# Kernel optimization log

Measured on AMD Instinct MI355X. Metric: run time of the kernel, lower is better.

Reference implementation:

```python
import jax, jax.numpy as jnp
import numpy as np

MEM_DIM = 4000
FEATURES = 2048
THRESHOLD = 1.0 / MEM_DIM
EPS = 1e-12
COS_EPS = 1e-8  # torch CosineSimilarity default eps


def setup_inputs() -> dict:
    key = jax.random.key(0)
    k1, k2 = jax.random.split(key)
    x = jax.random.normal(k1, (8192, FEATURES), dtype=jnp.float32)
    # kaiming_uniform_ with a=0: bound = sqrt(6 / fan_in), fan_in = FEATURES
    bound = float(np.sqrt(6.0 / FEATURES))
    memory = jax.random.uniform(k2, (MEM_DIM, FEATURES), dtype=jnp.float32,
                                minval=-bound, maxval=bound)
    return {"x": x, "memory": memory}


def reference(x, memory):
    # Cosine similarity via normalized matmul: [b, MEM_DIM]
    z_norm = jnp.linalg.norm(x, axis=1)              # [b]
    m_norm = jnp.linalg.norm(memory, axis=1)         # [M]
    logits = (x @ memory.T) / jnp.maximum(z_norm[:, None] * m_norm[None, :], COS_EPS)
    w = jax.nn.softmax(logits, axis=1)               # [b, M]
    # sparse shrinkage: relu(w - t) * w / (|w - t| + eps)
    d = w - THRESHOLD
    w = jnp.maximum(d, 0.0) * w / (jnp.abs(d) + EPS)
    # L1 normalize over memory dim (F.normalize p=1, eps=1e-12)
    w = w / jnp.maximum(jnp.sum(jnp.abs(w), axis=1, keepdims=True), EPS)
    return w @ memory                                # [b, features]
```

## Files before the change

### kernel.cpp

```cpp
#include <hip/hip_runtime.h>
#include <hip/hip_fp16.h>
#include <math.h>

#define FEATURES 2048
#define MROWS 4000
#define NPAD 4096
#define BROWS 8192

typedef unsigned short u16;
typedef unsigned int u32;

typedef __attribute__((ext_vector_type(8))) _Float16 f16x8;
typedef __attribute__((ext_vector_type(8))) short s16x8;
typedef __attribute__((ext_vector_type(4))) float f32x4;

__device__ __forceinline__ u16 f2h(float f) {
  union { _Float16 h; u16 u; } cv;
  cv.h = (_Float16)f;
  return cv.u;
}
__device__ __forceinline__ u16 f2bf(float f) {
  u32 u = __float_as_uint(f);
  u32 r = (u + 0x7FFFu + ((u >> 16) & 1u)) >> 16;
  return (u16)r;
}
__device__ __forceinline__ float bf2f(u16 h) {
  return __uint_as_float(((u32)h) << 16);
}

#define GLD16(g, l)                                                            \
  __builtin_amdgcn_global_load_lds(                                            \
      (const __attribute__((address_space(1))) u32*)(g),                       \
      (__attribute__((address_space(3))) u32*)(l), 16, 0, 0)


__global__ __launch_bounds__(256) void conv_split_bf16_kernel(
    const float* __restrict__ src, u16* __restrict__ hi, u16* __restrict__ lo,
    float* __restrict__ norms, int nrows) {
  __shared__ float red[4];
  const int row = blockIdx.x;
  const int tid = threadIdx.x;
  ushort4* hp = (ushort4*)(hi + (size_t)row * FEATURES);
  ushort4* lp = (ushort4*)(lo + (size_t)row * FEATURES);
  float ss = 0.f;
  if (row < nrows) {
    const float4* sp = (const float4*)(src + (size_t)row * FEATURES);
#pragma unroll
    for (int p = 0; p < 2; ++p) {
      const int idx = tid + p * 256;
      float4 f = sp[idx];
      ushort4 h, l;
      h.x = f2bf(f.x); l.x = f2bf(f.x - bf2f(h.x)); ss += f.x * f.x;
      h.y = f2bf(f.y); l.y = f2bf(f.y - bf2f(h.y)); ss += f.y * f.y;
      h.z = f2bf(f.z); l.z = f2bf(f.z - bf2f(h.z)); ss += f.z * f.z;
      h.w = f2bf(f.w); l.w = f2bf(f.w - bf2f(h.w)); ss += f.w * f.w;
      hp[idx] = h;
      lp[idx] = l;
    }
  } else {
    const ushort4 zz = {0, 0, 0, 0};
#pragma unroll
    for (int p = 0; p < 2; ++p) {
      hp[tid + p * 256] = zz;
      lp[tid + p * 256] = zz;
    }
  }
#pragma unroll
  for (int o = 32; o; o >>= 1) ss += __shfl_xor(ss, o);
  if ((tid & 63) == 0) red[tid >> 6] = ss;
  __syncthreads();
  if (tid == 0) {
    float tot = red[0] + red[1] + red[2] + red[3];
    norms[row] = (row < nrows) ? sqrtf(tot) : 1.0f;
  }
}

__global__ __launch_bounds__(256) void transpose_f16_kernel(
    const float* __restrict__ mem, u16* __restrict__ mt) {
  __shared__ float tile[64][65];
  const int tid = threadIdx.x;
  const int ti = blockIdx.x;
  const int tj = blockIdx.y;
  const int c = tid & 63;
  const int r0 = tid >> 6;
#pragma unroll
  for (int i = 0; i < 16; ++i) {
    const int r = i * 4 + r0;
    const int gr = ti * 64 + r;
    float v = 0.f;
    if (gr < MROWS) v = mem[(size_t)gr * FEATURES + tj * 64 + c];
    tile[r][c] = v;
  }
  __syncthreads();
#pragma unroll
  for (int i = 0; i < 16; ++i) {
    const int r = i * 4 + r0;
    mt[(size_t)(tj * 64 + r) * NPAD + ti * 64 + c] = f2h(tile[c][r]);
  }
}

__global__ __launch_bounds__(512, 2) void gemm1_kernel(
    const u16* __restrict__ Ah, const u16* __restrict__ Al,
    const u16* __restrict__ Bh, const u16* __restrict__ Bl,
    const float* __restrict__ zn, const float* __restrict__ mn,
    float* __restrict__ C) {
  __shared__ __align__(16) u16 sAh[2 * 8192];
  __shared__ __align__(16) u16 sAl[2 * 8192];
  __shared__ __align__(16) u16 sBh[2 * 8192];
  __shared__ __align__(16) u16 sBl[2 * 8192];
  const int tid = threadIdx.x;
  const int wid = tid >> 6;
  const int lane = tid & 63;
  const int brow = blockIdx.x * 256;
  const int bcol = blockIdx.y * 256;
  const int wr = wid >> 2;
  const int wc = wid & 3;
  const int fr = lane & 15, fq = lane >> 4;
  const int fqa = (fq ^ ((fr >> 1) & 3)) * 8;

  f32x4 acc[8][4];
#pragma unroll
  for (int m = 0; m < 8; ++m)
#pragma unroll
    for (int n = 0; n < 4; ++n) acc[m][n] = (f32x4){0.f, 0.f, 0.f, 0.f};

  const int r_st = tid >> 2;
  const int c_sw = (((tid & 3) ^ ((tid >> 3) & 3)) << 3);

#define STAGE1(cur, k0)                                                        \
  {                                                                            \
    _Pragma("unroll") for (int p = 0; p < 2; ++p) {                            \
      const int r = r_st + p * 128;                                            \
      const size_t offA = (size_t)(brow + r) * FEATURES + ((k0) + c_sw);       \
      const size_t offB = (size_t)(bcol + r) * FEATURES + ((k0) + c_sw);       \
      const int ldso = (cur) * 8192 + p * 4096 + wid * 512;                    \
      GLD16(Ah + offA, sAh + ldso);                                            \
      GLD16(Al + offA, sAl + ldso);                                            \
      GLD16(Bh + offB, sBh + ldso);                                            \
      GLD16(Bl + offB, sBl + ldso);                                            \
    }                                                                          \
  }

  STAGE1(0, 0);
  __syncthreads();
  for (int kt = 0; kt < 64; ++kt) {
    const int cur = kt & 1;
    const int bo = cur * 8192;
    s16x8 bh[4], bl[4];
#pragma unroll
    for (int n = 0; n < 4; ++n) {
      const int ro = bo + (wc * 64 + n * 16 + fr) * 32 + fqa;
      bh[n] = *(const s16x8*)(sBh + ro);
      bl[n] = *(const s16x8*)(sBl + ro);
    }
    s16x8 ah[8], al[8];
#pragma unroll
    for (int m = 0; m < 8; ++m) {
      const int ro = bo + (wr * 128 + m * 16 + fr) * 32 + fqa;
      ah[m] = *(const s16x8*)(sAh + ro);
      al[m] = *(const s16x8*)(sAl + ro);
    }
    if (kt < 63) STAGE1(cur ^ 1, (kt + 1) * 32);
#pragma unroll
    for (int m = 0; m < 8; ++m)
#pragma unroll
      for (int n = 0; n < 4; ++n) {
        acc[m][n] = __builtin_amdgcn_mfma_f32_16x16x32_bf16(
            ah[m], bh[n], acc[m][n], 0, 0, 0);
        acc[m][n] = __builtin_amdgcn_mfma_f32_16x16x32_bf16(
            al[m], bh[n], acc[m][n], 0, 0, 0);
        acc[m][n] = __builtin_amdgcn_mfma_f32_16x16x32_bf16(
            ah[m], bl[n], acc[m][n], 0, 0, 0);
      }
    __syncthreads();
  }
#undef STAGE1

#pragma unroll
  for (int m = 0; m < 8; ++m) {
#pragma unroll
    for (int r = 0; r < 4; ++r) {
      const int row = brow + wr * 128 + m * 16 + fq * 4 + r;
      const float z = zn[row];
#pragma unroll
      for (int n = 0; n < 4; ++n) {
        const int col = bcol + wc * 64 + n * 16 + fr;
        const float denom = fmaxf(z * mn[col], 1e-8f);
        C[(size_t)row * NPAD + col] = acc[m][n][r] / denom;
      }
    }
  }
}

__global__ __launch_bounds__(256) void softmax_kernel(float* __restrict__ logits) {
  __shared__ float red[4];
  const int row = blockIdx.x;
  const int tid = threadIdx.x;
  const float* lp = logits + (size_t)row * NPAD;
  u16* W = (u16*)logits + (size_t)row * (2 * NPAD);
  float v[16];
  float lmax = -3.4e38f;
#pragma unroll
  for (int i = 0; i < 16; ++i) {
    const int c = tid + i * 256;
    v[i] = (c < MROWS) ? lp[c] : -3.4e38f;
    lmax = fmaxf(lmax, v[i]);
  }
#pragma unroll
  for (int o = 32; o; o >>= 1) lmax = fmaxf(lmax, __shfl_xor(lmax, o));
  if ((tid & 63) == 0) red[tid >> 6] = lmax;
  __syncthreads();
  lmax = fmaxf(fmaxf(red[0], red[1]), fmaxf(red[2], red[3]));

  float s = 0.f;
#pragma unroll
  for (int i = 0; i < 16; ++i) {
    const int c = tid + i * 256;
    if (c < MROWS) {
      v[i] = expf(v[i] - lmax);
      s += v[i];
    } else {
      v[i] = 0.f;
    }
  }
#pragma unroll
  for (int o = 32; o; o >>= 1) s += __shfl_xor(s, o);
  __syncthreads();
  if ((tid & 63) == 0) red[tid >> 6] = s;
  __syncthreads();
  const float Z = red[0] + red[1] + red[2] + red[3];

  const float THR = (float)(1.0 / 4000.0);
  float s2 = 0.f;
#pragma unroll
  for (int i = 0; i < 16; ++i) {
    float w = v[i] / Z;
    const float d = w - THR;
    w = fmaxf(d, 0.f) * w / (fabsf(d) + 1e-12f);
    v[i] = w;
    s2 += w;
  }
#pragma unroll
  for (int o = 32; o; o >>= 1) s2 += __shfl_xor(s2, o);
  __syncthreads();
  if ((tid & 63) == 0) red[tid >> 6] = s2;
  __syncthreads();
  const float S = fmaxf(red[0] + red[1] + red[2] + red[3], 1e-12f);

#pragma unroll
  for (int i = 0; i < 16; ++i) {
    const int c = tid + i * 256;
    W[c] = f2h(v[i] / S);
  }
}

__global__ __launch_bounds__(256) void gemm2_kernel(
    const u16* __restrict__ A, const u16* __restrict__ B,
    float* __restrict__ C) {
  __shared__ __align__(16) u16 sA[2 * 4096];
  __shared__ __align__(16) u16 sB[2 * 4096];
  const int tid = threadIdx.x;
  const int wid = tid >> 6;
  const int lane = tid & 63;
  const int brow = blockIdx.x * 128;
  const int bcol = blockIdx.y * 128;
  const int wr = wid >> 1, wc = wid & 1;
  const int fr = lane & 15, fq = lane >> 4;
  const int fqa = (fq ^ ((fr >> 1) & 3)) * 8;

  f32x4 acc[4][4];
#pragma unroll
  for (int m = 0; m < 4; ++m)
#pragma unroll
    for (int n = 0; n < 4; ++n) acc[m][n] = (f32x4){0.f, 0.f, 0.f, 0.f};

  const int r_st = tid >> 2;
  const int c_sw = (((tid & 3) ^ ((tid >> 3) & 3)) << 3);

#define STAGE2(cur, k0)                                                        \
  {                                                                            \
    _Pragma("unroll") for (int p = 0; p < 2; ++p) {                            \
      const int r = r_st + p * 64;                                             \
      const size_t offA = (size_t)(brow + r) * (2 * NPAD) + ((k0) + c_sw);     \
      const size_t offB = (size_t)(bcol + r) * NPAD + ((k0) + c_sw);           \
      const int ldso = (cur) * 4096 + p * 2048 + wid * 512;                    \
      GLD16(A + offA, sA + ldso);                                              \
      GLD16(B + offB, sB + ldso);                                              \
    }                                                                          \
  }

#define G2_COMPUTE(cur)                                                        \
  {                                                                            \
    const int bo = (cur) * 4096;                                               \
    f16x8 af[4], bf[4];                                                        \
    _Pragma("unroll") for (int m = 0; m < 4; ++m)                              \
      af[m] = *(const f16x8*)(sA + bo + (wr * 64 + m * 16 + fr) * 32 + fqa);   \
    _Pragma("unroll") for (int n = 0; n < 4; ++n)                              \
      bf[n] = *(const f16x8*)(sB + bo + (wc * 64 + n * 16 + fr) * 32 + fqa);   \
    _Pragma("unroll") for (int m = 0; m < 4; ++m)                              \
      _Pragma("unroll") for (int n = 0; n < 4; ++n)                            \
        acc[m][n] = __builtin_amdgcn_mfma_f32_16x16x32_f16(                    \
            af[m], bf[n], acc[m][n], 0, 0, 0);                                 \
  }

  STAGE2(0, 0);
  __syncthreads();
  for (int kt = 0; kt < 128; ++kt) {
    const int cur = kt & 1;
    if (kt < 127) STAGE2(cur ^ 1, (kt + 1) * 32);
    G2_COMPUTE(cur);
    __syncthreads();
  }
#undef STAGE2
#undef G2_COMPUTE

#pragma unroll
  for (int m = 0; m < 4; ++m) {
#pragma unroll
    for (int r = 0; r < 4; ++r) {
      const int row = brow + wr * 64 + m * 16 + fq * 4 + r;
#pragma unroll
      for (int n = 0; n < 4; ++n) {
        const int col = bcol + wc * 64 + n * 16 + fr;
        C[(size_t)row * FEATURES + col] = acc[m][n][r];
      }
    }
  }
}

extern "C" void kernel_launch(void* const* d_in, const int* in_sizes, int n_in,
                              void* d_out, int out_size, void* d_ws, size_t ws_size,
                              hipStream_t stream) {
  const float* x = (const float*)d_in[0];
  const float* mem = (const float*)d_in[1];
  float* out = (float*)d_out;
  char* ws = (char*)d_ws;

  size_t o = 0;
  u16* mh = (u16*)(ws + o); o += (size_t)NPAD * FEATURES * 2;
  u16* ml = (u16*)(ws + o); o += (size_t)NPAD * FEATURES * 2;
  u16* mt = (u16*)(ws + o); o += (size_t)FEATURES * NPAD * 2;
  float* zn = (float*)(ws + o); o += (size_t)BROWS * 4;
  float* mn = (float*)(ws + o); o += (size_t)NPAD * 4;
  const size_t base = o;

  int CH = BROWS;
  size_t need = 0;
  for (;; CH >>= 1) {
    need = base + (size_t)CH * FEATURES * 2 * 2 + (size_t)CH * NPAD * 4;
    if (need <= ws_size || CH == 256) break;
  }
  if (need > ws_size) return;
  u16* xh = (u16*)(ws + base);
  u16* xl = (u16*)(ws + base + (size_t)CH * FEATURES * 2);
  float* lg = (float*)(ws + base + (size_t)CH * FEATURES * 4);

  conv_split_bf16_kernel<<<NPAD, 256, 0, stream>>>(mem, mh, ml, mn, MROWS);
  transpose_f16_kernel<<<dim3(NPAD / 64, FEATURES / 64), 256, 0, stream>>>(mem, mt);

  for (int r0 = 0; r0 < BROWS; r0 += CH) {
    conv_split_bf16_kernel<<<CH, 256, 0, stream>>>(x + (size_t)r0 * FEATURES, xh, xl, zn, CH);
    gemm1_kernel<<<dim3(CH / 256, NPAD / 256), 512, 0, stream>>>(xh, xl, mh, ml, zn, mn, lg);
    softmax_kernel<<<CH, 256, 0, stream>>>(lg);
    gemm2_kernel<<<dim3(CH / 128, FEATURES / 128), 256, 0, stream>>>(
        (const u16*)lg, mt, out + (size_t)r0 * FEATURES);
  }
}
```

Before: 571.6 us.

## Enlarge gemm2 tile to 256x256 with 8 waves and hoist gemm1 load pointers

The gemm2 block tile grows from 128x128 with 4 waves to 256x256 with 8 waves, and each wave now computes a 128x64 sub-tile. This is meant to raise arithmetic intensity and cut global and LDS traffic per FLOP. In gemm1, global load addresses are precomputed as pointers that advance by 32 each k-step, replacing per-stage 64-bit offset math. The larger tile uses more LDS and accumulator registers, and launch_bounds(512,2) may cause register pressure or spills. The grid also shrinks to 256 blocks per chunk, which may underfill the GPU.

```diff
diff --git a/kernel.cpp b/kernel.cpp
--- a/kernel.cpp
+++ b/kernel.cpp
@@ -127,21 +127,31 @@
   const int r_st = tid >> 2;
   const int c_sw = (((tid & 3) ^ ((tid >> 3) & 3)) << 3);
 
-#define STAGE1(cur, k0)                                                        \
+  const u16* pA0 = Ah + (size_t)(brow + r_st) * FEATURES + c_sw;
+  const u16* pA1 = pA0 + 128 * FEATURES;
+  const u16* pL0 = Al + (size_t)(brow + r_st) * FEATURES + c_sw;
+  const u16* pL1 = pL0 + 128 * FEATURES;
+  const u16* pB0 = Bh + (size_t)(bcol + r_st) * FEATURES + c_sw;
+  const u16* pB1 = pB0 + 128 * FEATURES;
+  const u16* pM0 = Bl + (size_t)(bcol + r_st) * FEATURES + c_sw;
+  const u16* pM1 = pM0 + 128 * FEATURES;
+
+#define STAGE1(cur)                                                            \
   {                                                                            \
-    _Pragma("unroll") for (int p = 0; p < 2; ++p) {                            \
-      const int r = r_st + p * 128;                                            \
-      const size_t offA = (size_t)(brow + r) * FEATURES + ((k0) + c_sw);       \
-      const size_t offB = (size_t)(bcol + r) * FEATURES + ((k0) + c_sw);       \
-      const int ldso = (cur) * 8192 + p * 4096 + wid * 512;                    \
-      GLD16(Ah + offA, sAh + ldso);                                            \
-      GLD16(Al + offA, sAl + ldso);                                            \
-      GLD16(Bh + offB, sBh + ldso);                                            \
-      GLD16(Bl + offB, sBl + ldso);                                            \
-    }                                                                          \
-  }
-
-  STAGE1(0, 0);
+    const int l0 = (cur) * 8192 + wid * 512;                                   \
+    GLD16(pA0, sAh + l0);                                                      \
+    GLD16(pL0, sAl + l0);                                                      \
+    GLD16(pB0, sBh + l0);                                                      \
+    GLD16(pM0, sBl + l0);                                                      \
+    GLD16(pA1, sAh + l0 + 4096);                                               \
+    GLD16(pL1, sAl + l0 + 4096);                                               \
+    GLD16(pB1, sBh + l0 + 4096);                                               \
+    GLD16(pM1, sBl + l0 + 4096);                                               \
+    pA0 += 32; pA1 += 32; pL0 += 32; pL1 += 32;                                \
+    pB0 += 32; pB1 += 32; pM0 += 32; pM1 += 32;                                \
+  }
+
+  STAGE1(0);
   __syncthreads();
   for (int kt = 0; kt < 64; ++kt) {
     const int cur = kt & 1;
@@ -160,7 +170,7 @@
       ah[m] = *(const s16x8*)(sAh + ro);
       al[m] = *(const s16x8*)(sAl + ro);
     }
-    if (kt < 63) STAGE1(cur ^ 1, (kt + 1) * 32);
+    if (kt < 63) STAGE1(cur ^ 1);
 #pragma unroll
     for (int m = 0; m < 8; ++m)
 #pragma unroll
@@ -254,23 +264,23 @@
   }
 }
 
-__global__ __launch_bounds__(256) void gemm2_kernel(
+__global__ __launch_bounds__(512, 2) void gemm2_kernel(
     const u16* __restrict__ A, const u16* __restrict__ B,
     float* __restrict__ C) {
-  __shared__ __align__(16) u16 sA[2 * 4096];
-  __shared__ __align__(16) u16 sB[2 * 4096];
+  __shared__ __align__(16) u16 sA[2 * 8192];
+  __shared__ __align__(16) u16 sB[2 * 8192];
   const int tid = threadIdx.x;
   const int wid = tid >> 6;
   const int lane = tid & 63;
-  const int brow = blockIdx.x * 128;
-  const int bcol = blockIdx.y * 128;
-  const int wr = wid >> 1, wc = wid & 1;
+  const int brow = blockIdx.x * 256;
+  const int bcol = blockIdx.y * 256;
+  const int wr = wid >> 2, wc = wid & 3;
   const int fr = lane & 15, fq = lane >> 4;
   const int fqa = (fq ^ ((fr >> 1) & 3)) * 8;
 
-  f32x4 acc[4][4];
-#pragma unroll
-  for (int m = 0; m < 4; ++m)
+  f32x4 acc[8][4];
+#pragma unroll
+  for (int m = 0; m < 8; ++m)
 #pragma unroll
     for (int n = 0; n < 4; ++n) acc[m][n] = (f32x4){0.f, 0.f, 0.f, 0.f};
 
@@ -280,10 +290,10 @@
 #define STAGE2(cur, k0)                                                        \
   {                                                                            \
     _Pragma("unroll") for (int p = 0; p < 2; ++p) {                            \
-      const int r = r_st + p * 64;                                             \
+      const int r = r_st + p * 128;                                            \
       const size_t offA = (size_t)(brow + r) * (2 * NPAD) + ((k0) + c_sw);     \
       const size_t offB = (size_t)(bcol + r) * NPAD + ((k0) + c_sw);           \
-      const int ldso = (cur) * 4096 + p * 2048 + wid * 512;                    \
+      const int ldso = (cur) * 8192 + p * 4096 + wid * 512;                    \
       GLD16(A + offA, sA + ldso);                                              \
       GLD16(B + offB, sB + ldso);                                              \
     }                                                                          \
@@ -291,16 +301,17 @@
 
 #define G2_COMPUTE(cur)                                                        \
   {                                                                            \
-    const int bo = (cur) * 4096;                                               \
-    f16x8 af[4], bf[4];                                                        \
-    _Pragma("unroll") for (int m = 0; m < 4; ++m)                              \
-      af[m] = *(const f16x8*)(sA + bo + (wr * 64 + m * 16 + fr) * 32 + fqa);   \
+    const int bo = (cur) * 8192;                                               \
+    f16x8 bf[4];                                                               \
     _Pragma("unroll") for (int n = 0; n < 4; ++n)                              \
       bf[n] = *(const f16x8*)(sB + bo + (wc * 64 + n * 16 + fr) * 32 + fqa);   \
-    _Pragma("unroll") for (int m = 0; m < 4; ++m)                              \
+    _Pragma("unroll") for (int m = 0; m < 8; ++m) {                            \
+      const f16x8 af =                                                         \
+          *(const f16x8*)(sA + bo + (wr * 128 + m * 16 + fr) * 32 + fqa);      \
       _Pragma("unroll") for (int n = 0; n < 4; ++n)                            \
         acc[m][n] = __builtin_amdgcn_mfma_f32_16x16x32_f16(                    \
-            af[m], bf[n], acc[m][n], 0, 0, 0);                                 \
+            af, bf[n], acc[m][n], 0, 0, 0);                                    \
+    }                                                                          \
   }
 
   STAGE2(0, 0);
@@ -315,10 +326,10 @@
 #undef G2_COMPUTE
 
 #pragma unroll
-  for (int m = 0; m < 4; ++m) {
+  for (int m = 0; m < 8; ++m) {
 #pragma unroll
     for (int r = 0; r < 4; ++r) {
-      const int row = brow + wr * 64 + m * 16 + fq * 4 + r;
+      const int row = brow + wr * 128 + m * 16 + fq * 4 + r;
 #pragma unroll
       for (int n = 0; n < 4; ++n) {
         const int col = bcol + wc * 64 + n * 16 + fr;
@@ -362,7 +373,7 @@
     conv_split_bf16_kernel<<<CH, 256, 0, stream>>>(x + (size_t)r0 * FEATURES, xh, xl, zn, CH);
     gemm1_kernel<<<dim3(CH / 256, NPAD / 256), 512, 0, stream>>>(xh, xl, mh, ml, zn, mn, lg);
     softmax_kernel<<<CH, 256, 0, stream>>>(lg);
-    gemm2_kernel<<<dim3(CH / 128, FEATURES / 128), 256, 0, stream>>>(
+    gemm2_kernel<<<dim3(CH / 256, FEATURES / 256), 512, 0, stream>>>(
         (const u16*)lg, mt, out + (size_t)r0 * FEATURES);
   }
 }
```

After: 558.0 us. -2.4%, faster.
